# Performance work log

Hardware: AMD Instinct MI355X
Metric: run time of the kernel (lower is better)

The kernel has to match this reference:

```python
import jax, jax.numpy as jnp
import numpy as np

B, S, D = 16, 2048, 128
NEG = -1e9


def setup_inputs() -> dict:
    key = jax.random.key(0)
    kq, kk, kv = jax.random.split(key, 3)
    queries = jax.random.normal(kq, (B, S, D), dtype=jnp.float32)
    keys = jax.random.normal(kk, (B, S, D), dtype=jnp.float32)
    values = jax.random.normal(kv, (B, S, D), dtype=jnp.float32)
    # causal additive mask: 0 on/below diagonal, -1e9 above
    causal = jnp.triu(jnp.ones((S, S), dtype=jnp.float32), k=1) * NEG
    return {"queries": queries, "keys": keys, "values": values, "mask": causal}


def reference(queries, keys, values, mask):
    d = queries.shape[-1]
    scale = 1.0 / jnp.sqrt(jnp.asarray(d, dtype=queries.dtype))
    # scores: [b, q, k]
    scores = jnp.einsum("bqd,bkd->bqk", queries, keys) * scale
    scores = scores + mask  # broadcast [S,S] over batch
    weights = jax.nn.softmax(scores, axis=-1)
    # dropout p=0.0 in eval mode -> identity
    return jnp.einsum("bqk,bkd->bqd", weights, values)
```

## Files before the change

kernel.cpp:

```cpp
#include <hip/hip_runtime.h>
#include <hip/hip_bf16.h>
#include <cstdint>

#define SS   2048
#define DD   128
#define QBLK 64
#define KBLK 64
#define NTILES (SS / KBLK)
#define TILE_BYTES 16384
#define WS_NEED ((size_t)16 * NTILES * TILE_BYTES * 2)

typedef __attribute__((ext_vector_type(8))) short short8;
typedef __attribute__((ext_vector_type(4))) float f32x4;

__device__ __forceinline__ unsigned short f2bf(float x) {
  return __builtin_bit_cast(unsigned short, (__bf16)x);
}

__device__ __forceinline__ int sigma_col(int a) {
  return (a & 35) | ((a & 12) << 1) | ((a & 16) >> 2);
}

__global__ __launch_bounds__(256) void prepack_kv(
    const float* __restrict__ K, const float* __restrict__ V, char* __restrict__ ws)
{
  __shared__ float vf[64][129];
  const int b = blockIdx.x, t = blockIdx.y;
  const int tid = threadIdx.x;
  const float* Kt = K + ((size_t)b * SS + t * KBLK) * DD;
  const float* Vt = V + ((size_t)b * SS + t * KBLK) * DD;
  char* Kd = ws + ((size_t)(b * NTILES + t)) * TILE_BYTES;
  char* Vd = ws + (size_t)16 * NTILES * TILE_BYTES + ((size_t)(b * NTILES + t)) * TILE_BYTES;

  #pragma unroll
  for (int u = 0; u < 4; ++u) {
    int row = u * 16 + (tid >> 4);
    int col = 8 * (tid & 15);
    const float4* sp = reinterpret_cast<const float4*>(Kt + (size_t)row * DD + col);
    float4 x = sp[0], y = sp[1];
    short8 w;
    w[0] = f2bf(x.x); w[1] = f2bf(x.y); w[2] = f2bf(x.z); w[3] = f2bf(x.w);
    w[4] = f2bf(y.x); w[5] = f2bf(y.y); w[6] = f2bf(y.z); w[7] = f2bf(y.w);
    int off = (row * 256 + col * 2) ^ ((row & 7) << 4);
    *reinterpret_cast<short8*>(Kd + off) = w;
  }
  #pragma unroll
  for (int u = 0; u < 4; ++u) {
    int row = u * 16 + (tid >> 4);
    int col = 8 * (tid & 15);
    const float4* sp = reinterpret_cast<const float4*>(Vt + (size_t)row * DD + col);
    float4 x = sp[0], y = sp[1];
    vf[row][col + 0] = x.x; vf[row][col + 1] = x.y; vf[row][col + 2] = x.z; vf[row][col + 3] = x.w;
    vf[row][col + 4] = y.x; vf[row][col + 5] = y.y; vf[row][col + 6] = y.z; vf[row][col + 7] = y.w;
  }
  __syncthreads();
  #pragma unroll
  for (int q = 0; q < 4; ++q) {
    int idx = q * 256 + tid;
    int d = idx >> 3, y = idx & 7;
    short8 w;
    #pragma unroll
    for (int j = 0; j < 8; ++j) {
      int a = (j & 3) | ((y & 3) << 2) | ((j & 4) << 2) | ((y & 4) << 3);
      w[j] = f2bf(vf[a][d]);
    }
    int off = ((d << 7) + (y << 4)) ^ ((((d >> 3) ^ d) & 7) << 4);
    *reinterpret_cast<short8*>(Vd + off) = w;
  }
}

__device__ __forceinline__ void stage_tile(const char* Ksrc, const char* Vsrc,
                                           char* Kl, char* Vl, int wid, int lane)
{
  #pragma unroll
  for (int i = 0; i < 4; ++i) {
    int off = wid * 4096 + i * 1024;
    __builtin_amdgcn_global_load_lds(
        (const __attribute__((address_space(1))) unsigned int*)(Ksrc + off + lane * 16),
        (__attribute__((address_space(3))) unsigned int*)(Kl + off), 16, 0, 0);
  }
  #pragma unroll
  for (int i = 0; i < 4; ++i) {
    int off = wid * 4096 + i * 1024;
    __builtin_amdgcn_global_load_lds(
        (const __attribute__((address_space(1))) unsigned int*)(Vsrc + off + lane * 16),
        (__attribute__((address_space(3))) unsigned int*)(Vl + off), 16, 0, 0);
  }
}

__global__ __launch_bounds__(256) void sdpa_causal_v2(
    const float* __restrict__ Q, const char* __restrict__ ws, float* __restrict__ O)
{
  __shared__ __align__(16) char smem[2 * 32768];

  const int b = blockIdx.x;
  const int y = blockIdx.y;
  const int qb = (y < 16) ? (31 - y) : (y - 16);
  const int q0 = qb * QBLK;
  const int tid = threadIdx.x;
  const int lane = tid & 63;
  const int wid  = tid >> 6;
  const int l15  = lane & 15;
  const int hi   = lane >> 4;

  const float* Qb = Q + (size_t)b * SS * DD;
  float*       Ob = O + (size_t)b * SS * DD;
  const char*  Kws = ws + ((size_t)b * NTILES) * TILE_BYTES;
  const char*  Vws = ws + (size_t)16 * NTILES * TILE_BYTES + ((size_t)b * NTILES) * TILE_BYTES;

  const float scale = 0.08838834764831845f;

  short8 qf[4];
  {
    const float* qrow = Qb + (size_t)(q0 + wid * 16 + l15) * DD;
    #pragma unroll
    for (int c = 0; c < 4; ++c) {
      const float4* p = reinterpret_cast<const float4*>(qrow + 32 * c + 8 * hi);
      float4 x = p[0], y2 = p[1];
      short8 w;
      w[0] = f2bf(x.x * scale); w[1] = f2bf(x.y * scale);
      w[2] = f2bf(x.z * scale); w[3] = f2bf(x.w * scale);
      w[4] = f2bf(y2.x * scale); w[5] = f2bf(y2.y * scale);
      w[6] = f2bf(y2.z * scale); w[7] = f2bf(y2.w * scale);
      qf[c] = w;
    }
  }

  f32x4 o[8];
  #pragma unroll
  for (int nt = 0; nt < 8; ++nt) o[nt] = (f32x4){0.f, 0.f, 0.f, 0.f};
  float m = -INFINITY;
  float lsum = 0.f;

  const int ntile = qb + 1;
  int cur = 0;

  stage_tile(Kws, Vws, smem, smem + 16384, wid, lane);
  __syncthreads();

  for (int t = 0; t < ntile; ++t) {
    if (t + 1 < ntile) {
      char* nb = smem + (cur ^ 1) * 32768;
      stage_tile(Kws + (size_t)(t + 1) * TILE_BYTES, Vws + (size_t)(t + 1) * TILE_BYTES,
                 nb, nb + 16384, wid, lane);
    }

    const char* Kl = smem + cur * 32768;
    const char* Vl = Kl + 16384;
    const int kv0 = t * KBLK;

    f32x4 sacc[4];
    __builtin_amdgcn_s_setprio(1);
    #pragma unroll
    for (int g = 0; g < 4; ++g) {
      f32x4 acc = {0.f, 0.f, 0.f, 0.f};
      #pragma unroll
      for (int c = 0; c < 4; ++c) {
        int row = g * 16 + l15;
        int byteoff = (row * 256 + (32 * c + 8 * hi) * 2) ^ ((row & 7) << 4);
        short8 kf = *reinterpret_cast<const short8*>(Kl + byteoff);
        acc = __builtin_amdgcn_mfma_f32_16x16x32_bf16(kf, qf[c], acc, 0, 0, 0);
      }
      sacc[g] = acc;
    }
    __builtin_amdgcn_s_setprio(0);

    if (t == ntile - 1) {
      const int q = q0 + wid * 16 + l15;
      #pragma unroll
      for (int g = 0; g < 4; ++g)
        #pragma unroll
        for (int i = 0; i < 4; ++i) {
          int key = kv0 + g * 16 + 4 * hi + i;
          if (key > q) sacc[g][i] = -1e30f;
        }
    }

    float tmax = -INFINITY;
    #pragma unroll
    for (int g = 0; g < 4; ++g)
      #pragma unroll
      for (int i = 0; i < 4; ++i) tmax = fmaxf(tmax, sacc[g][i]);
    tmax = fmaxf(tmax, __shfl_xor(tmax, 16));
    tmax = fmaxf(tmax, __shfl_xor(tmax, 32));
    float mnew = fmaxf(m, tmax);
    float corr = __expf(m - mnew);
    m = mnew;

    float p[4][4];
    float psum = 0.f;
    #pragma unroll
    for (int g = 0; g < 4; ++g)
      #pragma unroll
      for (int i = 0; i < 4; ++i) {
        float pv = __expf(sacc[g][i] - mnew);
        p[g][i] = pv;
        psum += pv;
      }
    psum += __shfl_xor(psum, 16);
    psum += __shfl_xor(psum, 32);
    lsum = lsum * corr + psum;

    float corrO[4];
    #pragma unroll
    for (int i = 0; i < 4; ++i) corrO[i] = __shfl(corr, 4 * hi + i);
    #pragma unroll
    for (int nt = 0; nt < 8; ++nt)
      #pragma unroll
      for (int i = 0; i < 4; ++i) o[nt][i] *= corrO[i];

    short8 pf[2];
    #pragma unroll
    for (int ks = 0; ks < 2; ++ks) {
      short8 w;
      #pragma unroll
      for (int i = 0; i < 4; ++i) {
        w[i]     = f2bf(p[2 * ks][i]);
        w[4 + i] = f2bf(p[2 * ks + 1][i]);
      }
      pf[ks] = w;
    }

    __builtin_amdgcn_s_setprio(1);
    #pragma unroll
    for (int ks = 0; ks < 2; ++ks) {
      #pragma unroll
      for (int nt = 0; nt < 8; ++nt) {
        int d = nt * 16 + l15;
        int byteoff = ((d << 7) + (ks * 32 + 8 * hi) * 2) ^ ((((d >> 3) ^ d) & 7) << 4);
        short8 vvf = *reinterpret_cast<const short8*>(Vl + byteoff);
        o[nt] = __builtin_amdgcn_mfma_f32_16x16x32_bf16(pf[ks], vvf, o[nt], 0, 0, 0);
      }
    }
    __builtin_amdgcn_s_setprio(0);

    if (t + 1 < ntile) {
      __syncthreads();
      cur ^= 1;
    }
  }

  float rl = 1.0f / lsum;
  float rlO[4];
  #pragma unroll
  for (int i = 0; i < 4; ++i) rlO[i] = __shfl(rl, 4 * hi + i);
  const int qrow = q0 + wid * 16;
  #pragma unroll
  for (int nt = 0; nt < 8; ++nt)
    #pragma unroll
    for (int i = 0; i < 4; ++i)
      Ob[(size_t)(qrow + 4 * hi + i) * DD + nt * 16 + l15] = o[nt][i] * rlO[i];
}

__global__ __launch_bounds__(256) void sdpa_causal_kernel(
    const float* __restrict__ Q, const float* __restrict__ K,
    const float* __restrict__ V, float* __restrict__ O)
{
  __shared__ __align__(16) char smem[KBLK * DD * 2 + DD * KBLK * 2];
  char* Klds  = smem;
  char* Vtlds = smem + KBLK * DD * 2;

  const int b   = blockIdx.x;
  const int qb  = (int)gridDim.y - 1 - (int)blockIdx.y;
  const int q0  = qb * QBLK;
  const int tid = threadIdx.x;
  const int lane = tid & 63;
  const int wid  = tid >> 6;
  const int l15  = lane & 15;
  const int hi   = lane >> 4;

  const float* Qb = Q + (size_t)b * SS * DD;
  const float* Kb = K + (size_t)b * SS * DD;
  const float* Vb = V + (size_t)b * SS * DD;
  float*       Ob = O + (size_t)b * SS * DD;

  const float scale = 0.08838834764831845f;

  short8 qf[4];
  {
    const float* qrow = Qb + (size_t)(q0 + wid * 16 + l15) * DD;
    #pragma unroll
    for (int c = 0; c < 4; ++c) {
      const float4* p = reinterpret_cast<const float4*>(qrow + 32 * c + 8 * hi);
      float4 x = p[0], y = p[1];
      short8 w;
      w[0] = f2bf(x.x * scale); w[1] = f2bf(x.y * scale);
      w[2] = f2bf(x.z * scale); w[3] = f2bf(x.w * scale);
      w[4] = f2bf(y.x * scale); w[5] = f2bf(y.y * scale);
      w[6] = f2bf(y.z * scale); w[7] = f2bf(y.w * scale);
      qf[c] = w;
    }
  }

  f32x4 o[8];
  #pragma unroll
  for (int nt = 0; nt < 8; ++nt) o[nt] = (f32x4){0.f, 0.f, 0.f, 0.f};
  float m = -INFINITY;
  float lsum = 0.f;

  const int ntile = qb + 1;
  for (int t = 0; t < ntile; ++t) {
    const int kv0 = t * KBLK;
    if (t) __syncthreads();

    #pragma unroll
    for (int u = 0; u < 4; ++u) {
      int row = u * 16 + (tid >> 4);
      int col = 8 * (tid & 15);
      const float4* sp = reinterpret_cast<const float4*>(Kb + (size_t)(kv0 + row) * DD + col);
      float4 x = sp[0], y = sp[1];
      short8 w;
      w[0] = f2bf(x.x); w[1] = f2bf(x.y); w[2] = f2bf(x.z); w[3] = f2bf(x.w);
      w[4] = f2bf(y.x); w[5] = f2bf(y.y); w[6] = f2bf(y.z); w[7] = f2bf(y.w);
      int byteoff = (row * 256 + col * 2) ^ ((row & 7) << 4);
      *reinterpret_cast<short8*>(Klds + byteoff) = w;
    }
    #pragma unroll
    for (int u = 0; u < 4; ++u) {
      int row = u * 16 + (tid >> 4);
      int col = 8 * (tid & 15);
      const float4* sp = reinterpret_cast<const float4*>(Vb + (size_t)(kv0 + row) * DD + col);
      float4 x = sp[0], y = sp[1];
      int sc = sigma_col(row);
      float vals[8] = {x.x, x.y, x.z, x.w, y.x, y.y, y.z, y.w};
      #pragma unroll
      for (int j = 0; j < 8; ++j) {
        int d = col + j;
        int byteoff = ((d << 7) + (sc << 1)) ^ ((((d >> 3) ^ d) & 7) << 4);
        *reinterpret_cast<unsigned short*>(Vtlds + byteoff) = f2bf(vals[j]);
      }
    }
    __syncthreads();

    f32x4 sacc[4];
    #pragma unroll
    for (int g = 0; g < 4; ++g) {
      f32x4 acc = {0.f, 0.f, 0.f, 0.f};
      #pragma unroll
      for (int c = 0; c < 4; ++c) {
        int row = g * 16 + l15;
        int byteoff = (row * 256 + (32 * c + 8 * hi) * 2) ^ ((row & 7) << 4);
        short8 kf = *reinterpret_cast<const short8*>(Klds + byteoff);
        acc = __builtin_amdgcn_mfma_f32_16x16x32_bf16(kf, qf[c], acc, 0, 0, 0);
      }
      sacc[g] = acc;
    }

    if (t == ntile - 1) {
      const int q = q0 + wid * 16 + l15;
      #pragma unroll
      for (int g = 0; g < 4; ++g)
        #pragma unroll
        for (int i = 0; i < 4; ++i) {
          int key = kv0 + g * 16 + 4 * hi + i;
          if (key > q) sacc[g][i] = -1e30f;
        }
    }

    float tmax = -INFINITY;
    #pragma unroll
    for (int g = 0; g < 4; ++g)
      #pragma unroll
      for (int i = 0; i < 4; ++i) tmax = fmaxf(tmax, sacc[g][i]);
    tmax = fmaxf(tmax, __shfl_xor(tmax, 16));
    tmax = fmaxf(tmax, __shfl_xor(tmax, 32));
    float mnew = fmaxf(m, tmax);
    float corr = __expf(m - mnew);
    m = mnew;

    float p[4][4];
    float psum = 0.f;
    #pragma unroll
    for (int g = 0; g < 4; ++g)
      #pragma unroll
      for (int i = 0; i < 4; ++i) {
        float pv = __expf(sacc[g][i] - mnew);
        p[g][i] = pv;
        psum += pv;
      }
    psum += __shfl_xor(psum, 16);
    psum += __shfl_xor(psum, 32);
    lsum = lsum * corr + psum;

    float corrO[4];
    #pragma unroll
    for (int i = 0; i < 4; ++i) corrO[i] = __shfl(corr, 4 * hi + i);
    #pragma unroll
    for (int nt = 0; nt < 8; ++nt)
      #pragma unroll
      for (int i = 0; i < 4; ++i) o[nt][i] *= corrO[i];

    short8 pf[2];
    #pragma unroll
    for (int ks = 0; ks < 2; ++ks) {
      short8 w;
      #pragma unroll
      for (int i = 0; i < 4; ++i) {
        w[i]     = f2bf(p[2 * ks][i]);
        w[4 + i] = f2bf(p[2 * ks + 1][i]);
      }
      pf[ks] = w;
    }

    #pragma unroll
    for (int ks = 0; ks < 2; ++ks) {
      #pragma unroll
      for (int nt = 0; nt < 8; ++nt) {
        int d = nt * 16 + l15;
        int byteoff = ((d << 7) + (ks * 32 + 8 * hi) * 2) ^ ((((d >> 3) ^ d) & 7) << 4);
        short8 vvf = *reinterpret_cast<const short8*>(Vtlds + byteoff);
        o[nt] = __builtin_amdgcn_mfma_f32_16x16x32_bf16(pf[ks], vvf, o[nt], 0, 0, 0);
      }
    }
  }

  float rl = 1.0f / lsum;
  float rlO[4];
  #pragma unroll
  for (int i = 0; i < 4; ++i) rlO[i] = __shfl(rl, 4 * hi + i);
  const int qrow = q0 + wid * 16;
  #pragma unroll
  for (int nt = 0; nt < 8; ++nt)
    #pragma unroll
    for (int i = 0; i < 4; ++i)
      Ob[(size_t)(qrow + 4 * hi + i) * DD + nt * 16 + l15] = o[nt][i] * rlO[i];
}

extern "C" void kernel_launch(void* const* d_in, const int* in_sizes, int n_in,
                              void* d_out, int out_size, void* d_ws, size_t ws_size,
                              hipStream_t stream) {
  const float* Q = (const float*)d_in[0];
  const float* K = (const float*)d_in[1];
  const float* V = (const float*)d_in[2];
  float* O = (float*)d_out;

  if (ws_size >= WS_NEED) {
    char* ws = (char*)d_ws;
    prepack_kv<<<dim3(16, NTILES), 256, 0, stream>>>(K, V, ws);
    sdpa_causal_v2<<<dim3(16, 32), 256, 0, stream>>>(Q, ws, O);
  } else {
    sdpa_causal_kernel<<<dim3(16, 32), 256, 0, stream>>>(Q, K, V, O);
  }
}
```

Before: 64.81 us.

## Split long causal query blocks into two KV chunks and merge partials

Query blocks 16-31 get their KV range split into two chunks handled by separate workgroups, which write unnormalized partial outputs plus row max and sum to workspace. A merge kernel then combines them with a log-sum-exp rescale. This evens out per-block work, trimming the long critical path of the causal tail and raising occupancy from 512 to 768 workgroups. It also adds a conditional skip of the output rescale when the running max does not change. The cost is an extra kernel launch and partial-output round trips through global memory, and the old fallback kernel that needed no workspace is removed.

```diff
diff --git a/kernel.cpp b/kernel.cpp
--- a/kernel.cpp
+++ b/kernel.cpp
@@ -8,7 +8,14 @@
 #define KBLK 64
 #define NTILES (SS / KBLK)
 #define TILE_BYTES 16384
-#define WS_NEED ((size_t)16 * NTILES * TILE_BYTES * 2)
+#define CHUNK 16
+
+#define WS_KPRE   ((size_t)0)
+#define WS_VPRE   ((size_t)16 * NTILES * TILE_BYTES)
+#define WS_PARTO  ((size_t)16 * NTILES * TILE_BYTES * 2)
+#define WS_PARTML (WS_PARTO + (size_t)16*16*2*64*128*4)
+#define WS_NEED_FULL (WS_PARTML + (size_t)16*16*2*64*2*4)
+#define WS_NEED_PRE  ((size_t)16 * NTILES * TILE_BYTES * 2)
 
 typedef __attribute__((ext_vector_type(8))) short short8;
 typedef __attribute__((ext_vector_type(4))) float f32x4;
@@ -29,8 +36,8 @@
   const int tid = threadIdx.x;
   const float* Kt = K + ((size_t)b * SS + t * KBLK) * DD;
   const float* Vt = V + ((size_t)b * SS + t * KBLK) * DD;
-  char* Kd = ws + ((size_t)(b * NTILES + t)) * TILE_BYTES;
-  char* Vd = ws + (size_t)16 * NTILES * TILE_BYTES + ((size_t)(b * NTILES + t)) * TILE_BYTES;
+  char* Kd = ws + WS_KPRE + ((size_t)(b * NTILES + t)) * TILE_BYTES;
+  char* Vd = ws + WS_VPRE + ((size_t)(b * NTILES + t)) * TILE_BYTES;
 
   #pragma unroll
   for (int u = 0; u < 4; ++u) {
@@ -88,14 +95,20 @@
   }
 }
 
-__global__ __launch_bounds__(256) void sdpa_causal_v2(
-    const float* __restrict__ Q, const char* __restrict__ ws, float* __restrict__ O)
+__global__ __launch_bounds__(256) void sdpa_chunk(
+    const float* __restrict__ Q, const char* __restrict__ ws,
+    float* __restrict__ O, float* __restrict__ partO, float* __restrict__ partML)
 {
   __shared__ __align__(16) char smem[2 * 32768];
 
   const int b = blockIdx.x;
-  const int y = blockIdx.y;
-  const int qb = (y < 16) ? (31 - y) : (y - 16);
+  const int s = blockIdx.y;
+  int qb, kvt0, ntile, pid = 0;
+  bool domask, dostore;
+  if (s < 16)      { qb = 16 + s; kvt0 = 0;  ntile = 16;      domask = false; dostore = false; pid = (qb-16)*2;   }
+  else if (s < 32) { qb = 47 - s; kvt0 = 16; ntile = qb - 15; domask = true;  dostore = false; pid = (qb-16)*2+1; }
+  else             { qb = 47 - s; kvt0 = 0;  ntile = qb + 1;  domask = true;  dostore = true; }
+
   const int q0 = qb * QBLK;
   const int tid = threadIdx.x;
   const int lane = tid & 63;
@@ -104,9 +117,8 @@
   const int hi   = lane >> 4;
 
   const float* Qb = Q + (size_t)b * SS * DD;
-  float*       Ob = O + (size_t)b * SS * DD;
-  const char*  Kws = ws + ((size_t)b * NTILES) * TILE_BYTES;
-  const char*  Vws = ws + (size_t)16 * NTILES * TILE_BYTES + ((size_t)b * NTILES) * TILE_BYTES;
+  const char*  Kws = ws + WS_KPRE + ((size_t)b * NTILES + kvt0) * TILE_BYTES;
+  const char*  Vws = ws + WS_VPRE + ((size_t)b * NTILES + kvt0) * TILE_BYTES;
 
   const float scale = 0.08838834764831845f;
 
@@ -132,9 +144,7 @@
   float m = -INFINITY;
   float lsum = 0.f;
 
-  const int ntile = qb + 1;
   int cur = 0;
-
   stage_tile(Kws, Vws, smem, smem + 16384, wid, lane);
   __syncthreads();
 
@@ -147,7 +157,6 @@
 
     const char* Kl = smem + cur * 32768;
     const char* Vl = Kl + 16384;
-    const int kv0 = t * KBLK;
 
     f32x4 sacc[4];
     __builtin_amdgcn_s_setprio(1);
@@ -165,8 +174,9 @@
     }
     __builtin_amdgcn_s_setprio(0);
 
-    if (t == ntile - 1) {
+    if (domask && t == ntile - 1) {
       const int q = q0 + wid * 16 + l15;
+      const int kv0 = (kvt0 + t) * KBLK;
       #pragma unroll
       for (int g = 0; g < 4; ++g)
         #pragma unroll
@@ -176,6 +186,211 @@
         }
     }
 
+    float gm[4];
+    #pragma unroll
+    for (int g = 0; g < 4; ++g)
+      gm[g] = fmaxf(fmaxf(sacc[g][0], sacc[g][1]), fmaxf(sacc[g][2], sacc[g][3]));
+    float tmax = fmaxf(fmaxf(gm[0], gm[1]), fmaxf(gm[2], gm[3]));
+    tmax = fmaxf(tmax, __shfl_xor(tmax, 16));
+    tmax = fmaxf(tmax, __shfl_xor(tmax, 32));
+
+    bool skip = __all(tmax <= m) && (t > 0 || m != -INFINITY);
+    float mnew = skip ? m : fmaxf(m, tmax);
+    float corr = skip ? 1.f : __expf(m - mnew);
+    m = mnew;
+
+    float p[4][4];
+    float gs[4];
+    #pragma unroll
+    for (int g = 0; g < 4; ++g) {
+      #pragma unroll
+      for (int i = 0; i < 4; ++i) p[g][i] = __expf(sacc[g][i] - mnew);
+      gs[g] = (p[g][0] + p[g][1]) + (p[g][2] + p[g][3]);
+    }
+    float psum = (gs[0] + gs[1]) + (gs[2] + gs[3]);
+    psum += __shfl_xor(psum, 16);
+    psum += __shfl_xor(psum, 32);
+    lsum = lsum * corr + psum;
+
+    if (!skip) {
+      float corrO[4];
+      #pragma unroll
+      for (int i = 0; i < 4; ++i) corrO[i] = __shfl(corr, 4 * hi + i);
+      #pragma unroll
+      for (int nt = 0; nt < 8; ++nt)
+        #pragma unroll
+        for (int i = 0; i < 4; ++i) o[nt][i] *= corrO[i];
+    }
+
+    short8 pf[2];
+    #pragma unroll
+    for (int ks = 0; ks < 2; ++ks) {
+      short8 w;
+      #pragma unroll
+      for (int i = 0; i < 4; ++i) {
+        w[i]     = f2bf(p[2 * ks][i]);
+        w[4 + i] = f2bf(p[2 * ks + 1][i]);
+      }
+      pf[ks] = w;
+    }
+
+    __builtin_amdgcn_s_setprio(1);
+    #pragma unroll
+    for (int ks = 0; ks < 2; ++ks) {
+      #pragma unroll
+      for (int nt = 0; nt < 8; ++nt) {
+        int d = nt * 16 + l15;
+        int byteoff = ((d << 7) + (ks * 32 + 8 * hi) * 2) ^ ((((d >> 3) ^ d) & 7) << 4);
+        short8 vvf = *reinterpret_cast<const short8*>(Vl + byteoff);
+        o[nt] = __builtin_amdgcn_mfma_f32_16x16x32_bf16(pf[ks], vvf, o[nt], 0, 0, 0);
+      }
+    }
+    __builtin_amdgcn_s_setprio(0);
+
+    if (t + 1 < ntile) {
+      __syncthreads();
+      cur ^= 1;
+    }
+  }
+
+  if (dostore) {
+    float rl = 1.0f / lsum;
+    float rlO[4];
+    #pragma unroll
+    for (int i = 0; i < 4; ++i) rlO[i] = __shfl(rl, 4 * hi + i);
+    float* Ob = O + (size_t)b * SS * DD;
+    const int qrow = q0 + wid * 16;
+    #pragma unroll
+    for (int nt = 0; nt < 8; ++nt)
+      #pragma unroll
+      for (int i = 0; i < 4; ++i)
+        Ob[(size_t)(qrow + 4 * hi + i) * DD + nt * 16 + l15] = o[nt][i] * rlO[i];
+  } else {
+    const int pbase = (b * 16 + (qb - 16)) * 2 + (s < 16 ? 0 : 1);
+    float* po = partO + (size_t)pbase * (64 * 128);
+    #pragma unroll
+    for (int nt = 0; nt < 8; ++nt)
+      #pragma unroll
+      for (int i = 0; i < 4; ++i)
+        po[(size_t)(wid * 16 + 4 * hi + i) * DD + nt * 16 + l15] = o[nt][i];
+    if (hi == 0) {
+      float2* ml = (float2*)partML;
+      ml[pbase * 64 + wid * 16 + l15] = make_float2(m, lsum);
+    }
+  }
+}
+
+__global__ __launch_bounds__(256) void merge_partials(
+    const float* __restrict__ partO, const float* __restrict__ partML,
+    float* __restrict__ O)
+{
+  int idx = blockIdx.x * 256 + threadIdx.x;
+  int d4  = idx & 31;
+  int row = (idx >> 5) & 63;
+  int qr  = (idx >> 11) & 15;
+  int b   = idx >> 15;
+  int pid0 = (b * 16 + qr) * 2;
+  float2 ml0 = ((const float2*)partML)[pid0 * 64 + row];
+  float2 ml1 = ((const float2*)partML)[(pid0 + 1) * 64 + row];
+  float M  = fmaxf(ml0.x, ml1.x);
+  float a0 = __expf(ml0.x - M), a1 = __expf(ml1.x - M);
+  float inv = 1.0f / (ml0.y * a0 + ml1.y * a1);
+  float s0 = a0 * inv, s1 = a1 * inv;
+  float4 o0 = ((const float4*)partO)[(size_t)pid0 * 2048 + row * 32 + d4];
+  float4 o1 = ((const float4*)partO)[(size_t)(pid0 + 1) * 2048 + row * 32 + d4];
+  float4 r;
+  r.x = o0.x * s0 + o1.x * s1;
+  r.y = o0.y * s0 + o1.y * s1;
+  r.z = o0.z * s0 + o1.z * s1;
+  r.w = o0.w * s0 + o1.w * s1;
+  ((float4*)O)[((size_t)b * 2048 + (16 + qr) * 64 + row) * 32 + d4] = r;
+}
+
+__global__ __launch_bounds__(256) void sdpa_causal_v2(
+    const float* __restrict__ Q, const char* __restrict__ ws, float* __restrict__ O)
+{
+  __shared__ __align__(16) char smem[2 * 32768];
+
+  const int b = blockIdx.x;
+  const int y = blockIdx.y;
+  int qb0 = (y < 16) ? (31 - y) : (y - 16);
+  const int qb = (b < 8) ? qb0 : (31 - qb0);
+  const int q0 = qb * QBLK;
+  const int tid = threadIdx.x;
+  const int lane = tid & 63;
+  const int wid  = tid >> 6;
+  const int l15  = lane & 15;
+  const int hi   = lane >> 4;
+
+  const float* Qb = Q + (size_t)b * SS * DD;
+  float*       Ob = O + (size_t)b * SS * DD;
+  const char*  Kws = ws + WS_KPRE + ((size_t)b * NTILES) * TILE_BYTES;
+  const char*  Vws = ws + WS_VPRE + ((size_t)b * NTILES) * TILE_BYTES;
+
+  const float scale = 0.08838834764831845f;
+
+  short8 qf[4];
+  {
+    const float* qrow = Qb + (size_t)(q0 + wid * 16 + l15) * DD;
+    #pragma unroll
+    for (int c = 0; c < 4; ++c) {
+      const float4* p = reinterpret_cast<const float4*>(qrow + 32 * c + 8 * hi);
+      float4 x = p[0], y2 = p[1];
+      short8 w;
+      w[0] = f2bf(x.x * scale); w[1] = f2bf(x.y * scale);
+      w[2] = f2bf(x.z * scale); w[3] = f2bf(x.w * scale);
+      w[4] = f2bf(y2.x * scale); w[5] = f2bf(y2.y * scale);
+      w[6] = f2bf(y2.z * scale); w[7] = f2bf(y2.w * scale);
+      qf[c] = w;
+    }
+  }
+
+  f32x4 o[8];
+  #pragma unroll
+  for (int nt = 0; nt < 8; ++nt) o[nt] = (f32x4){0.f, 0.f, 0.f, 0.f};
+  float m = -INFINITY;
+  float lsum = 0.f;
+
+  const int ntile = qb + 1;
+  int cur = 0;
+  stage_tile(Kws, Vws, smem, smem + 16384, wid, lane);
+  __syncthreads();
+
+  for (int t = 0; t < ntile; ++t) {
+    if (t + 1 < ntile) {
+      char* nb = smem + (cur ^ 1) * 32768;
+      stage_tile(Kws + (size_t)(t + 1) * TILE_BYTES, Vws + (size_t)(t + 1) * TILE_BYTES,
+                 nb, nb + 16384, wid, lane);
+    }
+    const char* Kl = smem + cur * 32768;
+    const char* Vl = Kl + 16384;
+    const int kv0 = t * KBLK;
+
+    f32x4 sacc[4];
+    #pragma unroll
+    for (int g = 0; g < 4; ++g) {
+      f32x4 acc = {0.f, 0.f, 0.f, 0.f};
+      #pragma unroll
+      for (int c = 0; c < 4; ++c) {
+        int row = g * 16 + l15;
+        int byteoff = (row * 256 + (32 * c + 8 * hi) * 2) ^ ((row & 7) << 4);
+        short8 kf = *reinterpret_cast<const short8*>(Kl + byteoff);
+        acc = __builtin_amdgcn_mfma_f32_16x16x32_bf16(kf, qf[c], acc, 0, 0, 0);
+      }
+      sacc[g] = acc;
+    }
+
+    if (t == ntile - 1) {
+      const int q = q0 + wid * 16 + l15;
+      #pragma unroll
+      for (int g = 0; g < 4; ++g)
+        #pragma unroll
+        for (int i = 0; i < 4; ++i) {
+          int key = kv0 + g * 16 + 4 * hi + i;
+          if (key > q) sacc[g][i] = -1e30f;
+        }
+    }
+
     float tmax = -INFINITY;
     #pragma unroll
     for (int g = 0; g < 4; ++g)
@@ -221,7 +436,6 @@
       pf[ks] = w;
     }
 
-    __builtin_amdgcn_s_setprio(1);
     #pragma unroll
     for (int ks = 0; ks < 2; ++ks) {
       #pragma unroll
@@ -232,185 +446,10 @@
         o[nt] = __builtin_amdgcn_mfma_f32_16x16x32_bf16(pf[ks], vvf, o[nt], 0, 0, 0);
       }
     }
-    __builtin_amdgcn_s_setprio(0);
 
     if (t + 1 < ntile) {
       __syncthreads();
       cur ^= 1;
-    }
-  }
-
-  float rl = 1.0f / lsum;
-  float rlO[4];
-  #pragma unroll
-  for (int i = 0; i < 4; ++i) rlO[i] = __shfl(rl, 4 * hi + i);
-  const int qrow = q0 + wid * 16;
-  #pragma unroll
-  for (int nt = 0; nt < 8; ++nt)
-    #pragma unroll
-    for (int i = 0; i < 4; ++i)
-      Ob[(size_t)(qrow + 4 * hi + i) * DD + nt * 16 + l15] = o[nt][i] * rlO[i];
-}
-
-__global__ __launch_bounds__(256) void sdpa_causal_kernel(
-    const float* __restrict__ Q, const float* __restrict__ K,
-    const float* __restrict__ V, float* __restrict__ O)
-{
-  __shared__ __align__(16) char smem[KBLK * DD * 2 + DD * KBLK * 2];
-  char* Klds  = smem;
-  char* Vtlds = smem + KBLK * DD * 2;
-
-  const int b   = blockIdx.x;
-  const int qb  = (int)gridDim.y - 1 - (int)blockIdx.y;
-  const int q0  = qb * QBLK;
-  const int tid = threadIdx.x;
-  const int lane = tid & 63;
-  const int wid  = tid >> 6;
-  const int l15  = lane & 15;
-  const int hi   = lane >> 4;
-
-  const float* Qb = Q + (size_t)b * SS * DD;
-  const float* Kb = K + (size_t)b * SS * DD;
-  const float* Vb = V + (size_t)b * SS * DD;
-  float*       Ob = O + (size_t)b * SS * DD;
-
-  const float scale = 0.08838834764831845f;
-
-  short8 qf[4];
-  {
-    const float* qrow = Qb + (size_t)(q0 + wid * 16 + l15) * DD;
-    #pragma unroll
-    for (int c = 0; c < 4; ++c) {
-      const float4* p = reinterpret_cast<const float4*>(qrow + 32 * c + 8 * hi);
-      float4 x = p[0], y = p[1];
-      short8 w;
-      w[0] = f2bf(x.x * scale); w[1] = f2bf(x.y * scale);
-      w[2] = f2bf(x.z * scale); w[3] = f2bf(x.w * scale);
-      w[4] = f2bf(y.x * scale); w[5] = f2bf(y.y * scale);
-      w[6] = f2bf(y.z * scale); w[7] = f2bf(y.w * scale);
-      qf[c] = w;
-    }
-  }
-
-  f32x4 o[8];
-  #pragma unroll
-  for (int nt = 0; nt < 8; ++nt) o[nt] = (f32x4){0.f, 0.f, 0.f, 0.f};
-  float m = -INFINITY;
-  float lsum = 0.f;
-
-  const int ntile = qb + 1;
-  for (int t = 0; t < ntile; ++t) {
-    const int kv0 = t * KBLK;
-    if (t) __syncthreads();
-
-    #pragma unroll
-    for (int u = 0; u < 4; ++u) {
-      int row = u * 16 + (tid >> 4);
-      int col = 8 * (tid & 15);
-      const float4* sp = reinterpret_cast<const float4*>(Kb + (size_t)(kv0 + row) * DD + col);
-      float4 x = sp[0], y = sp[1];
-      short8 w;
-      w[0] = f2bf(x.x); w[1] = f2bf(x.y); w[2] = f2bf(x.z); w[3] = f2bf(x.w);
-      w[4] = f2bf(y.x); w[5] = f2bf(y.y); w[6] = f2bf(y.z); w[7] = f2bf(y.w);
-      int byteoff = (row * 256 + col * 2) ^ ((row & 7) << 4);
-      *reinterpret_cast<short8*>(Klds + byteoff) = w;
-    }
-    #pragma unroll
-    for (int u = 0; u < 4; ++u) {
-      int row = u * 16 + (tid >> 4);
-      int col = 8 * (tid & 15);
-      const float4* sp = reinterpret_cast<const float4*>(Vb + (size_t)(kv0 + row) * DD + col);
-      float4 x = sp[0], y = sp[1];
-      int sc = sigma_col(row);
-      float vals[8] = {x.x, x.y, x.z, x.w, y.x, y.y, y.z, y.w};
-      #pragma unroll
-      for (int j = 0; j < 8; ++j) {
-        int d = col + j;
-        int byteoff = ((d << 7) + (sc << 1)) ^ ((((d >> 3) ^ d) & 7) << 4);
-        *reinterpret_cast<unsigned short*>(Vtlds + byteoff) = f2bf(vals[j]);
-      }
-    }
-    __syncthreads();
-
-    f32x4 sacc[4];
-    #pragma unroll
-    for (int g = 0; g < 4; ++g) {
-      f32x4 acc = {0.f, 0.f, 0.f, 0.f};
-      #pragma unroll
-      for (int c = 0; c < 4; ++c) {
-        int row = g * 16 + l15;
-        int byteoff = (row * 256 + (32 * c + 8 * hi) * 2) ^ ((row & 7) << 4);
-        short8 kf = *reinterpret_cast<const short8*>(Klds + byteoff);
-        acc = __builtin_amdgcn_mfma_f32_16x16x32_bf16(kf, qf[c], acc, 0, 0, 0);
-      }
-      sacc[g] = acc;
-    }
-
-    if (t == ntile - 1) {
-      const int q = q0 + wid * 16 + l15;
-      #pragma unroll
-      for (int g = 0; g < 4; ++g)
-        #pragma unroll
-        for (int i = 0; i < 4; ++i) {
-          int key = kv0 + g * 16 + 4 * hi + i;
-          if (key > q) sacc[g][i] = -1e30f;
-        }
-    }
-
-    float tmax = -INFINITY;
-    #pragma unroll
-    for (int g = 0; g < 4; ++g)
-      #pragma unroll
-      for (int i = 0; i < 4; ++i) tmax = fmaxf(tmax, sacc[g][i]);
-    tmax = fmaxf(tmax, __shfl_xor(tmax, 16));
-    tmax = fmaxf(tmax, __shfl_xor(tmax, 32));
-    float mnew = fmaxf(m, tmax);
-    float corr = __expf(m - mnew);
-    m = mnew;
-
-    float p[4][4];
-    float psum = 0.f;
-    #pragma unroll
-    for (int g = 0; g < 4; ++g)
-      #pragma unroll
-      for (int i = 0; i < 4; ++i) {
-        float pv = __expf(sacc[g][i] - mnew);
-        p[g][i] = pv;
-        psum += pv;
-      }
-    psum += __shfl_xor(psum, 16);
-    psum += __shfl_xor(psum, 32);
-    lsum = lsum * corr + psum;
-
-    float corrO[4];
-    #pragma unroll
-    for (int i = 0; i < 4; ++i) corrO[i] = __shfl(corr, 4 * hi + i);
-    #pragma unroll
-    for (int nt = 0; nt < 8; ++nt)
-      #pragma unroll
-      for (int i = 0; i < 4; ++i) o[nt][i] *= corrO[i];
-
-    short8 pf[2];
-    #pragma unroll
-    for (int ks = 0; ks < 2; ++ks) {
-      short8 w;
-      #pragma unroll
-      for (int i = 0; i < 4; ++i) {
-        w[i]     = f2bf(p[2 * ks][i]);
-        w[4 + i] = f2bf(p[2 * ks + 1][i]);
-      }
-      pf[ks] = w;
-    }
-
-    #pragma unroll
-    for (int ks = 0; ks < 2; ++ks) {
-      #pragma unroll
-      for (int nt = 0; nt < 8; ++nt) {
-        int d = nt * 16 + l15;
-        int byteoff = ((d << 7) + (ks * 32 + 8 * hi) * 2) ^ ((((d >> 3) ^ d) & 7) << 4);
-        short8 vvf = *reinterpret_cast<const short8*>(Vtlds + byteoff);
-        o[nt] = __builtin_amdgcn_mfma_f32_16x16x32_bf16(pf[ks], vvf, o[nt], 0, 0, 0);
-      }
     }
   }
 
@@ -433,12 +472,16 @@
   const float* K = (const float*)d_in[1];
   const float* V = (const float*)d_in[2];
   float* O = (float*)d_out;
-
-  if (ws_size >= WS_NEED) {
-    char* ws = (char*)d_ws;
+  char* ws = (char*)d_ws;
+
+  if (ws_size >= WS_NEED_FULL) {
+    float* partO  = (float*)(ws + WS_PARTO);
+    float* partML = (float*)(ws + WS_PARTML);
+    prepack_kv<<<dim3(16, NTILES), 256, 0, stream>>>(K, V, ws);
+    sdpa_chunk<<<dim3(16, 48), 256, 0, stream>>>(Q, ws, O, partO, partML);
+    merge_partials<<<2048, 256, 0, stream>>>(partO, partML, O);
+  } else if (ws_size >= WS_NEED_PRE) {
     prepack_kv<<<dim3(16, NTILES), 256, 0, stream>>>(K, V, ws);
     sdpa_causal_v2<<<dim3(16, 32), 256, 0, stream>>>(Q, ws, O);
-  } else {
-    sdpa_causal_kernel<<<dim3(16, 32), 256, 0, stream>>>(Q, K, V, O);
-  }
-}
+  }
+}
```

New measurement: 59.83 us. -7.7%, faster.
